# Performance work log

Hardware: AMD Instinct MI355X
Metric: run time of the kernel (lower is better)

Reference implementation:

```python
import jax, jax.numpy as jnp
import numpy as np

N_NODES = 100000
N_EDGES = 1600000
IN_DIM = 128
HID = 64
CONV2_OUT = 8
GLOBAL_DIM = 24
OUT_DIM = 1
NUM_GRAPHS = 64
NEG_SLOPE = 0.01


def setup_inputs() -> dict:
    key = jax.random.key(0)
    ks = jax.random.split(key, 12)
    x = jax.random.normal(ks[0], (N_NODES, IN_DIM), dtype=jnp.float32)
    edge_index = jax.random.randint(ks[1], (2, N_EDGES), 0, N_NODES, dtype=jnp.int32)
    batch = jnp.sort(jax.random.randint(ks[2], (N_NODES,), 0, NUM_GRAPHS, dtype=jnp.int32))
    global_features = jax.random.normal(ks[3], (NUM_GRAPHS, GLOBAL_DIM), dtype=jnp.float32)
    # GCNConv weights (glorot-ish scale) and Linear weights
    W1 = jax.random.normal(ks[4], (IN_DIM, HID), dtype=jnp.float32) / np.sqrt(IN_DIM)
    b1 = jnp.zeros((HID,), dtype=jnp.float32)
    W2 = jax.random.normal(ks[5], (HID, CONV2_OUT), dtype=jnp.float32) / np.sqrt(HID)
    b2 = jnp.zeros((CONV2_OUT,), dtype=jnp.float32)
    fcW1 = jax.random.normal(ks[6], (GLOBAL_DIM + CONV2_OUT, 16), dtype=jnp.float32) / np.sqrt(GLOBAL_DIM + CONV2_OUT)
    fcb1 = jnp.zeros((16,), dtype=jnp.float32)
    fcW2 = jax.random.normal(ks[7], (16, OUT_DIM), dtype=jnp.float32) / np.sqrt(16)
    fcb2 = jnp.zeros((OUT_DIM,), dtype=jnp.float32)
    return {"x": x, "edge_index": edge_index, "batch": batch,
            "global_features": global_features,
            "W1": W1, "b1": b1, "W2": W2, "b2": b2,
            "fcW1": fcW1, "fcb1": fcb1, "fcW2": fcW2, "fcb2": fcb2}


def gcn_conv(x, src, dst, W, b):
    """PyG GCNConv: add self-loops, sym-normalize, aggregate x@W from src->dst."""
    n = x.shape[0]
    h = x @ W  # [N, F_out]
    loop = jnp.arange(n, dtype=src.dtype)
    src2 = jnp.concatenate([src, loop])
    dst2 = jnp.concatenate([dst, loop])
    deg = jax.ops.segment_sum(jnp.ones_like(dst2, dtype=h.dtype), dst2, num_segments=n)
    dinv = jnp.where(deg > 0, jax.lax.rsqrt(deg), 0.0)
    norm = dinv[src2] * dinv[dst2]  # [E+N]
    msg = h[src2] * norm[:, None]   # edge gather (dominant traffic)
    out = jax.ops.segment_sum(msg, dst2, num_segments=n)
    return out + b


def reference(x, edge_index, batch, global_features, W1, b1, W2, b2, fcW1, fcb1, fcW2, fcb2):
    src, dst = edge_index[0], edge_index[1]
    h = jax.nn.leaky_relu(gcn_conv(x, src, dst, W1, b1), NEG_SLOPE)
    h = jax.nn.leaky_relu(gcn_conv(h, src, dst, W2, b2), NEG_SLOPE)
    # global mean pool over graphs
    sums = jax.ops.segment_sum(h, batch, num_segments=NUM_GRAPHS)
    cnts = jax.ops.segment_sum(jnp.ones((h.shape[0],), h.dtype), batch, num_segments=NUM_GRAPHS)
    pool = sums / jnp.maximum(cnts, 1.0)[:, None]
    z = jnp.concatenate([pool, global_features], axis=1)
    z = jax.nn.leaky_relu(z @ fcW1 + fcb1, NEG_SLOPE)
    z = jax.nn.leaky_relu(z @ fcW2 + fcb2, NEG_SLOPE)
    return z
```

## Files before the change

kernel.cpp:

```cpp
#include <hip/hip_runtime.h>

constexpr int N_NODES = 100000;
constexpr int N_EDGES = 1600000;
constexpr int IN_DIM  = 128;
constexpr int HID     = 64;
constexpr int C2      = 8;
constexpr int GDIM    = 24;
constexpr int NG      = 64;
constexpr float SLOPE = 0.01f;
constexpr int NB_SCAN = (N_NODES + 255) / 256;

__device__ __forceinline__ float lrelu(float v) { return v > 0.f ? v : SLOPE * v; }

__device__ __forceinline__ float bf2f(unsigned short u) {
    union { unsigned int i; float f; } c;
    c.i = ((unsigned int)u) << 16;
    return c.f;
}
__device__ __forceinline__ unsigned short f2bf(float f) {
    unsigned int i = __float_as_uint(f);
    unsigned int r = (i + 0x7fffu + ((i >> 16) & 1u)) >> 16;
    return (unsigned short)r;
}

__global__ void k_rank(const int* __restrict__ dst, int* __restrict__ deg,
                       int* __restrict__ rnk) {
    int e = blockIdx.x * 256 + threadIdx.x;
    if (e < N_EDGES) rnk[e] = atomicAdd(&deg[dst[e]], 1);
}

__global__ void k_scan1(const int* __restrict__ deg, int* __restrict__ rowptr,
                        int* __restrict__ bsum, float* __restrict__ dinv) {
    __shared__ int s[256];
    int tid = threadIdx.x;
    int i = blockIdx.x * 256 + tid;
    int v = (i < N_NODES) ? deg[i] : 0;
    if (i < N_NODES) dinv[i] = rsqrtf((float)(v + 1));
    s[tid] = v;
    __syncthreads();
    for (int off = 1; off < 256; off <<= 1) {
        int t = (tid >= off) ? s[tid - off] : 0;
        __syncthreads();
        s[tid] += t;
        __syncthreads();
    }
    if (i < N_NODES) rowptr[i] = s[tid] - v;
    if (tid == 255) bsum[blockIdx.x] = s[255];
}

__global__ void k_scan2(const int* __restrict__ bsum, int* __restrict__ bsumx) {
    __shared__ int s[512];
    int tid = threadIdx.x;
    int v = (tid < NB_SCAN) ? bsum[tid] : 0;
    s[tid] = v;
    __syncthreads();
    for (int off = 1; off < 512; off <<= 1) {
        int t = (tid >= off) ? s[tid - off] : 0;
        __syncthreads();
        s[tid] += t;
        __syncthreads();
    }
    if (tid < NB_SCAN) bsumx[tid] = s[tid] - v;
}

__global__ void k_place(const int* __restrict__ src, const int* __restrict__ dst,
                        const int* __restrict__ rnk, const int* __restrict__ rowptr,
                        const int* __restrict__ bsumx, int* __restrict__ eidx) {
    int e = blockIdx.x * 256 + threadIdx.x;
    if (e < N_EDGES) {
        int d = dst[e];
        eidx[rowptr[d] + bsumx[d >> 8] + rnk[e]] = src[e];
    }
}

__global__ __launch_bounds__(256) void k_gemm1(const float* __restrict__ x,
                                               const float* __restrict__ W1,
                                               const float* __restrict__ dinv,
                                               unsigned short* __restrict__ hs1) {
    __shared__ float sW[IN_DIM * HID];
    __shared__ float sX[32][IN_DIM];
    int node0 = blockIdx.x * 32;
    for (int t = threadIdx.x; t < IN_DIM * HID / 4; t += 256)
        ((float4*)sW)[t] = ((const float4*)W1)[t];
    for (int t = threadIdx.x; t < 32 * IN_DIM / 4; t += 256) {
        int r = t >> 5, c4 = t & 31;
        ((float4*)&sX[r][0])[c4] = ((const float4*)(x + (size_t)(node0 + r) * IN_DIM))[c4];
    }
    __syncthreads();
    int col = threadIdx.x & 63;
    int nb  = (threadIdx.x >> 6) * 8;
    float acc[8] = {0.f, 0.f, 0.f, 0.f, 0.f, 0.f, 0.f, 0.f};
    for (int k4 = 0; k4 < IN_DIM; k4 += 4) {
        float w0 = sW[(k4 + 0) * HID + col];
        float w1 = sW[(k4 + 1) * HID + col];
        float w2 = sW[(k4 + 2) * HID + col];
        float w3 = sW[(k4 + 3) * HID + col];
#pragma unroll
        for (int j = 0; j < 8; ++j) {
            float4 xv = *((const float4*)&sX[nb + j][k4]);
            acc[j] += xv.x * w0 + xv.y * w1 + xv.z * w2 + xv.w * w3;
        }
    }
#pragma unroll
    for (int j = 0; j < 8; ++j) {
        int n = node0 + nb + j;
        hs1[(size_t)n * HID + col] = f2bf(acc[j] * dinv[n]);
    }
}

__global__ __launch_bounds__(256) void k_agg1(const int* __restrict__ rowptr,
                                              const int* __restrict__ bsumx,
                                              const int* __restrict__ deg,
                                              const int* __restrict__ eidx,
                                              const unsigned short* __restrict__ hs1,
                                              const float* __restrict__ dinv,
                                              const float* __restrict__ b1,
                                              const float* __restrict__ W2,
                                              float* __restrict__ hs2) {
    int node = blockIdx.x * 4 + (threadIdx.x >> 6);
    int lane = threadIdx.x & 63;
    int q    = lane & 15;
    int slot = lane >> 4;
    int j0   = slot * 2;
    float w20[4], w21[4];
#pragma unroll
    for (int i = 0; i < 4; ++i) {
        w20[i] = W2[(4 * q + i) * C2 + j0];
        w21[i] = W2[(4 * q + i) * C2 + j0 + 1];
    }
    int start = rowptr[node] + bsumx[node >> 8];
    int cnt   = deg[node];
    float4 acc = make_float4(0.f, 0.f, 0.f, 0.f);
    for (int k = slot; k < cnt; k += 4) {
        int s = eidx[start + k];
        ushort4 v = ((const ushort4*)(hs1 + (size_t)s * HID))[q];
        acc.x += bf2f(v.x); acc.y += bf2f(v.y);
        acc.z += bf2f(v.z); acc.w += bf2f(v.w);
    }
    acc.x += __shfl_xor(acc.x, 16); acc.y += __shfl_xor(acc.y, 16);
    acc.z += __shfl_xor(acc.z, 16); acc.w += __shfl_xor(acc.w, 16);
    acc.x += __shfl_xor(acc.x, 32); acc.y += __shfl_xor(acc.y, 32);
    acc.z += __shfl_xor(acc.z, 32); acc.w += __shfl_xor(acc.w, 32);
    ushort4 hv = ((const ushort4*)(hs1 + (size_t)node * HID))[q];
    float  di = dinv[node];
    float4 bb = ((const float4*)b1)[q];
    float4 y;
    y.x = lrelu(di * (acc.x + bf2f(hv.x)) + bb.x);
    y.y = lrelu(di * (acc.y + bf2f(hv.y)) + bb.y);
    y.z = lrelu(di * (acc.z + bf2f(hv.z)) + bb.z);
    y.w = lrelu(di * (acc.w + bf2f(hv.w)) + bb.w);
    float p0 = y.x * w20[0] + y.y * w20[1] + y.z * w20[2] + y.w * w20[3];
    float p1 = y.x * w21[0] + y.y * w21[1] + y.z * w21[2] + y.w * w21[3];
#pragma unroll
    for (int m = 1; m < 16; m <<= 1) {
        p0 += __shfl_xor(p0, m);
        p1 += __shfl_xor(p1, m);
    }
    if (q == 0) {
        float2 r; r.x = p0 * di; r.y = p1 * di;
        ((float2*)(hs2 + (size_t)node * C2))[slot] = r;
    }
}

__global__ __launch_bounds__(256) void k_agg2(const int* __restrict__ rowptr,
                                              const int* __restrict__ bsumx,
                                              const int* __restrict__ deg,
                                              const int* __restrict__ eidx,
                                              const float* __restrict__ hs2,
                                              const float* __restrict__ dinv,
                                              const float* __restrict__ b2,
                                              float* __restrict__ y2) {
    int node = blockIdx.x * 4 + (threadIdx.x >> 6);
    int lane = threadIdx.x & 63;
    int q    = lane & 1;
    int slot = lane >> 1;
    int start = rowptr[node] + bsumx[node >> 8];
    int cnt   = deg[node];
    float4 acc = make_float4(0.f, 0.f, 0.f, 0.f);
    for (int k = slot; k < cnt; k += 32) {
        int s = eidx[start + k];
        float4 v = ((const float4*)(hs2 + (size_t)s * C2))[q];
        acc.x += v.x; acc.y += v.y; acc.z += v.z; acc.w += v.w;
    }
    for (int m = 2; m < 64; m <<= 1) {
        acc.x += __shfl_xor(acc.x, m); acc.y += __shfl_xor(acc.y, m);
        acc.z += __shfl_xor(acc.z, m); acc.w += __shfl_xor(acc.w, m);
    }
    if (slot == 0) {
        float4 h = ((const float4*)(hs2 + (size_t)node * C2))[q];
        float di = dinv[node];
        const float* bb = b2 + q * 4;
        float4 r;
        r.x = lrelu(di * (acc.x + h.x) + bb[0]);
        r.y = lrelu(di * (acc.y + h.y) + bb[1]);
        r.z = lrelu(di * (acc.z + h.z) + bb[2]);
        r.w = lrelu(di * (acc.w + h.w) + bb[3]);
        ((float4*)(y2 + (size_t)node * C2))[q] = r;
    }
}

__device__ __forceinline__ int lower_bound(const int* __restrict__ b, int n, int v) {
    int lo = 0, hi = n;
    while (lo < hi) {
        int m = (lo + hi) >> 1;
        if (b[m] < v) lo = m + 1; else hi = m;
    }
    return lo;
}

__global__ __launch_bounds__(256) void k_pool(const float* __restrict__ y2,
                                              const int* __restrict__ batch,
                                              const float* __restrict__ gfeat,
                                              const float* __restrict__ fcW1,
                                              const float* __restrict__ fcb1,
                                              const float* __restrict__ fcW2,
                                              const float* __restrict__ fcb2,
                                              float* __restrict__ out) {
    __shared__ float s[256];
    int g   = blockIdx.x;
    int tid = threadIdx.x;
    int start = lower_bound(batch, N_NODES, g);
    int end   = lower_bound(batch, N_NODES, g + 1);
    int col = tid & 7;
    float local = 0.f;
    for (int n = start + (tid >> 3); n < end; n += 32)
        local += y2[(size_t)n * C2 + col];
    s[tid] = local;
    __syncthreads();
    for (int off = 128; off >= 8; off >>= 1) {
        if (tid < off) s[tid] += s[tid + off];
        __syncthreads();
    }
    if (tid == 0) {
        float cnt = fmaxf((float)(end - start), 1.f);
        float z[C2 + GDIM];
        for (int c = 0; c < C2; ++c) z[c] = s[c] / cnt;
        for (int c = 0; c < GDIM; ++c) z[C2 + c] = gfeat[g * GDIM + c];
        float acc2 = fcb2[0];
        for (int j = 0; j < 16; ++j) {
            float acc = fcb1[j];
            for (int c = 0; c < C2 + GDIM; ++c) acc += z[c] * fcW1[c * 16 + j];
            acc2 += lrelu(acc) * fcW2[j];
        }
        out[g] = lrelu(acc2);
    }
}

extern "C" void kernel_launch(void* const* d_in, const int* in_sizes, int n_in,
                              void* d_out, int out_size, void* d_ws, size_t ws_size,
                              hipStream_t stream) {
    const float* x     = (const float*)d_in[0];
    const int*   ei    = (const int*)d_in[1];
    const int*   batch = (const int*)d_in[2];
    const float* gfeat = (const float*)d_in[3];
    const float* W1    = (const float*)d_in[4];
    const float* b1    = (const float*)d_in[5];
    const float* W2    = (const float*)d_in[6];
    const float* b2    = (const float*)d_in[7];
    const float* fcW1  = (const float*)d_in[8];
    const float* fcb1  = (const float*)d_in[9];
    const float* fcW2  = (const float*)d_in[10];
    const float* fcb2  = (const float*)d_in[11];
    const int* src = ei;
    const int* dst = ei + N_EDGES;

    char* ws = (char*)d_ws;
    size_t off = 0;
    auto alloc = [&](size_t bytes) -> void* {
        void* p = ws + off;
        off = (off + bytes + 255) & ~(size_t)255;
        return p;
    };
    int*   deg    = (int*)  alloc((size_t)N_NODES * 4);
    float* dinv   = (float*)alloc((size_t)N_NODES * 4);
    int*   rowptr = (int*)  alloc((size_t)N_NODES * 4);
    int*   bsum   = (int*)  alloc(512 * 4);
    int*   bsumx  = (int*)  alloc(512 * 4);
    int*   rnk    = (int*)  alloc((size_t)N_EDGES * 4);
    int*   eidx   = (int*)  alloc((size_t)N_EDGES * 4);
    unsigned short* hs1 = (unsigned short*)alloc((size_t)N_NODES * HID * 2);
    float* hs2    = (float*)alloc((size_t)N_NODES * C2 * 4);
    float* y2     = (float*)alloc((size_t)N_NODES * C2 * 4);

    hipMemsetAsync(deg, 0, (size_t)N_NODES * 4, stream);

    k_rank <<<(N_EDGES + 255) / 256, 256, 0, stream>>>(dst, deg, rnk);
    k_scan1<<<NB_SCAN, 256, 0, stream>>>(deg, rowptr, bsum, dinv);
    k_scan2<<<1, 512, 0, stream>>>(bsum, bsumx);
    k_place<<<(N_EDGES + 255) / 256, 256, 0, stream>>>(src, dst, rnk, rowptr, bsumx, eidx);

    k_gemm1<<<N_NODES / 32, 256, 0, stream>>>(x, W1, dinv, hs1);
    k_agg1 <<<N_NODES / 4, 256, 0, stream>>>(rowptr, bsumx, deg, eidx, hs1, dinv, b1, W2, hs2);
    k_agg2 <<<N_NODES / 4, 256, 0, stream>>>(rowptr, bsumx, deg, eidx, hs2, dinv, b2, y2);
    k_pool <<<NG, 256, 0, stream>>>(y2, batch, gfeat, fcW1, fcb1, fcW2, fcb2, (float*)d_out);
}
```

Measured before the change: 298.9 us.

## Use 16-byte bf16 gathers and shuffle-broadcast edge indices in aggregation kernels

In the first aggregation, each lane now loads 8 bf16 values (a uint4) per neighbour row instead of 4, so 8 lanes cover a row and 8 edges are processed per wave step instead of 4. Both aggregation kernels now load up to 64 edge indices with one coalesced load per wave and broadcast them with __shfl, replacing per-lane scattered index loads. The W2 projection and its reduction are reorganised to match the new lane mapping. This aims to raise memory-level parallelism and cut index-load traffic, at the cost of more registers and shuffle instructions.

```diff
diff --git a/kernel.cpp b/kernel.cpp
--- a/kernel.cpp
+++ b/kernel.cpp
@@ -12,11 +12,8 @@
 
 __device__ __forceinline__ float lrelu(float v) { return v > 0.f ? v : SLOPE * v; }
 
-__device__ __forceinline__ float bf2f(unsigned short u) {
-    union { unsigned int i; float f; } c;
-    c.i = ((unsigned int)u) << 16;
-    return c.f;
-}
+__device__ __forceinline__ float bflo(unsigned int u) { return __uint_as_float(u << 16); }
+__device__ __forceinline__ float bfhi(unsigned int u) { return __uint_as_float(u & 0xffff0000u); }
 __device__ __forceinline__ unsigned short f2bf(float f) {
     unsigned int i = __float_as_uint(f);
     unsigned int r = (i + 0x7fffu + ((i >> 16) & 1u)) >> 16;
@@ -119,47 +116,46 @@
                                               float* __restrict__ hs2) {
     int node = blockIdx.x * 4 + (threadIdx.x >> 6);
     int lane = threadIdx.x & 63;
-    int q    = lane & 15;
-    int slot = lane >> 4;
-    int j0   = slot * 2;
-    float w20[4], w21[4];
-#pragma unroll
-    for (int i = 0; i < 4; ++i) {
-        w20[i] = W2[(4 * q + i) * C2 + j0];
-        w21[i] = W2[(4 * q + i) * C2 + j0 + 1];
-    }
+    int q    = lane & 7;
+    int slot = lane >> 3;
+    float w2f[8];
+#pragma unroll
+    for (int i = 0; i < 8; ++i) w2f[i] = W2[(8 * q + i) * C2 + slot];
     int start = rowptr[node] + bsumx[node >> 8];
     int cnt   = deg[node];
-    float4 acc = make_float4(0.f, 0.f, 0.f, 0.f);
-    for (int k = slot; k < cnt; k += 4) {
-        int s = eidx[start + k];
-        ushort4 v = ((const ushort4*)(hs1 + (size_t)s * HID))[q];
-        acc.x += bf2f(v.x); acc.y += bf2f(v.y);
-        acc.z += bf2f(v.z); acc.w += bf2f(v.w);
-    }
-    acc.x += __shfl_xor(acc.x, 16); acc.y += __shfl_xor(acc.y, 16);
-    acc.z += __shfl_xor(acc.z, 16); acc.w += __shfl_xor(acc.w, 16);
-    acc.x += __shfl_xor(acc.x, 32); acc.y += __shfl_xor(acc.y, 32);
-    acc.z += __shfl_xor(acc.z, 32); acc.w += __shfl_xor(acc.w, 32);
-    ushort4 hv = ((const ushort4*)(hs1 + (size_t)node * HID))[q];
-    float  di = dinv[node];
-    float4 bb = ((const float4*)b1)[q];
-    float4 y;
-    y.x = lrelu(di * (acc.x + bf2f(hv.x)) + bb.x);
-    y.y = lrelu(di * (acc.y + bf2f(hv.y)) + bb.y);
-    y.z = lrelu(di * (acc.z + bf2f(hv.z)) + bb.z);
-    y.w = lrelu(di * (acc.w + bf2f(hv.w)) + bb.w);
-    float p0 = y.x * w20[0] + y.y * w20[1] + y.z * w20[2] + y.w * w20[3];
-    float p1 = y.x * w21[0] + y.y * w21[1] + y.z * w21[2] + y.w * w21[3];
-#pragma unroll
-    for (int m = 1; m < 16; m <<= 1) {
-        p0 += __shfl_xor(p0, m);
-        p1 += __shfl_xor(p1, m);
-    }
-    if (q == 0) {
-        float2 r; r.x = p0 * di; r.y = p1 * di;
-        ((float2*)(hs2 + (size_t)node * C2))[slot] = r;
-    }
+    float acc[8] = {0.f, 0.f, 0.f, 0.f, 0.f, 0.f, 0.f, 0.f};
+    for (int base = 0; base < cnt; base += 64) {
+        int idx = (base + lane < cnt) ? eidx[start + base + lane] : 0;
+        int lim = min(64, cnt - base);
+        for (int k = slot; k < lim; k += 8) {
+            int s = __shfl(idx, k);
+            uint4 v = ((const uint4*)(hs1 + (size_t)s * HID))[q];
+            acc[0] += bflo(v.x); acc[1] += bfhi(v.x);
+            acc[2] += bflo(v.y); acc[3] += bfhi(v.y);
+            acc[4] += bflo(v.z); acc[5] += bfhi(v.z);
+            acc[6] += bflo(v.w); acc[7] += bfhi(v.w);
+        }
+    }
+#pragma unroll
+    for (int m = 8; m < 64; m <<= 1)
+#pragma unroll
+        for (int i = 0; i < 8; ++i) acc[i] += __shfl_xor(acc[i], m);
+    uint4 hv = ((const uint4*)(hs1 + (size_t)node * HID))[q];
+    float self[8] = {bflo(hv.x), bfhi(hv.x), bflo(hv.y), bfhi(hv.y),
+                     bflo(hv.z), bfhi(hv.z), bflo(hv.w), bfhi(hv.w)};
+    float di = dinv[node];
+    float4 bb0 = ((const float4*)b1)[2 * q];
+    float4 bb1 = ((const float4*)b1)[2 * q + 1];
+    float bv[8] = {bb0.x, bb0.y, bb0.z, bb0.w, bb1.x, bb1.y, bb1.z, bb1.w};
+    float p = 0.f;
+#pragma unroll
+    for (int i = 0; i < 8; ++i) {
+        float y = lrelu(di * (acc[i] + self[i]) + bv[i]);
+        p += y * w2f[i];
+    }
+#pragma unroll
+    for (int m = 1; m < 8; m <<= 1) p += __shfl_xor(p, m);
+    if (q == 0) hs2[(size_t)node * C2 + slot] = p * di;
 }
 
 __global__ __launch_bounds__(256) void k_agg2(const int* __restrict__ rowptr,
@@ -177,10 +173,14 @@
     int start = rowptr[node] + bsumx[node >> 8];
     int cnt   = deg[node];
     float4 acc = make_float4(0.f, 0.f, 0.f, 0.f);
-    for (int k = slot; k < cnt; k += 32) {
-        int s = eidx[start + k];
-        float4 v = ((const float4*)(hs2 + (size_t)s * C2))[q];
-        acc.x += v.x; acc.y += v.y; acc.z += v.z; acc.w += v.w;
+    for (int base = 0; base < cnt; base += 64) {
+        int idx = (base + lane < cnt) ? eidx[start + base + lane] : 0;
+        int lim = min(64, cnt - base);
+        for (int k = slot; k < lim; k += 32) {
+            int s = __shfl(idx, k);
+            float4 v = ((const float4*)(hs2 + (size_t)s * C2))[q];
+            acc.x += v.x; acc.y += v.y; acc.z += v.z; acc.w += v.w;
+        }
     }
     for (int m = 2; m < 64; m <<= 1) {
         acc.x += __shfl_xor(acc.x, m); acc.y += __shfl_xor(acc.y, m);
```

New measurement: 278.5 us. 6.8% less time.
